# Kernel optimization log

Hardware: AMD Instinct MI355X
Metric: run time of the kernel (lower is better)

## Reference

```python
import jax, jax.numpy as jnp
import numpy as np

HIDDEN = 1024
INTER = 1408
N_EXPERTS = 8
TOTAL_TOKENS = 8192


def setup_inputs() -> dict:
    key = jax.random.key(0)
    k_x, k_w1, k_w2 = jax.random.split(key, 3)
    x = jax.random.normal(k_x, (TOTAL_TOKENS, HIDDEN), dtype=jnp.float32)
    # fused gate+up projection per expert: [E, H, 2*I]
    w1w3 = jax.random.normal(k_w1, (N_EXPERTS, HIDDEN, 2 * INTER), dtype=jnp.float32) * (HIDDEN ** -0.5)
    # down projection per expert: [E, I, H]
    w2 = jax.random.normal(k_w2, (N_EXPERTS, INTER, HIDDEN), dtype=jnp.float32) * (INTER ** -0.5)
    # deterministic uneven split that sums exactly to TOTAL_TOKENS
    tpe = np.array([700, 1300, 900, 1100, 1024, 1024, 800, 1344], dtype=np.int64)
    assert tpe.sum() == TOTAL_TOKENS
    tokens_per_expert = jnp.asarray(tpe)
    return {"x": x, "w1w3": w1w3, "w2": w2, "tokens_per_expert": tokens_per_expert, "decoding": False}


def _grouped_mm(inp, W, expert_ids):
    # inp: [T, D_in], W: [E, D_in, D_out]; rows of inp are grouped by expert,
    # expert_ids[t] = owning expert. Equivalent to per-segment GEMM with W[e].
    T = inp.shape[0]
    E = W.shape[0]
    out = jnp.zeros((T, W.shape[-1]), dtype=inp.dtype)
    for e in range(E):  # fixed small expert count; loop over experts, not tokens
        mask = (expert_ids == e)[:, None]
        out = out + jnp.where(mask, inp, 0.0) @ W[e]
    return out


def reference(x, w1w3, w2, tokens_per_expert, decoding):
    T = x.shape[0]
    E = w1w3.shape[0]
    # per-token expert id from contiguous segment lengths (jit-safe fixed length)
    expert_ids = jnp.repeat(jnp.arange(E), tokens_per_expert, total_repeat_length=T)
    gate_up = _grouped_mm(x, w1w3, expert_ids)          # [T, 2*I]
    gate, up = jnp.split(gate_up, 2, axis=-1)           # swiglu(split_dim=-1)
    h = jax.nn.silu(gate) * up                          # [T, I]
    return _grouped_mm(h, w2, expert_ids)               # [T, H]
```

## Files before the change

kernel.cpp:

```cpp
#include <hip/hip_runtime.h>
#include <hip/hip_bf16.h>


#define HIDDEN 1024
#define INTER  1408
#define NEXP   8
#define TOKENS 8192

typedef __attribute__((ext_vector_type(8))) short bf16x8;
typedef __attribute__((ext_vector_type(4))) float f32x4;
typedef __attribute__((ext_vector_type(4))) unsigned short u16x4;
typedef __attribute__((ext_vector_type(8))) unsigned short u16x8;

#define GLOAD_LDS16(g, l)                                                      \
  __builtin_amdgcn_global_load_lds(                                            \
      (const __attribute__((address_space(1))) void*)(g),                      \
      (__attribute__((address_space(3))) void*)(l), 16, 0, 0)

__device__ inline unsigned short f2bf(float f) {
  unsigned int x = __float_as_uint(f);
  x += 0x7fffu + ((x >> 16) & 1u);
  return (unsigned short)(x >> 16);
}

__device__ inline int detect_f32(const float* __restrict__ xf, int lane) {
  unsigned int u = __float_as_uint(xf[lane & 63]);
  int e = (u >> 23) & 0xff;
  return __popcll(__ballot(e >= 100 && e <= 140)) >= 48 ? 1 : 0;
}

__device__ inline void load_tpe(const int* __restrict__ raw, int* tpe) {
  bool ok = true; int s = 0;
#pragma unroll
  for (int e = 0; e < NEXP; e++) { int v = raw[e]; tpe[e] = v; ok = ok && (v >= 0 && v <= TOKENS); s += v; }
  if (ok && s == TOKENS) return;
  ok = true; s = 0;
#pragma unroll
  for (int e = 0; e < NEXP; e++) { int v = raw[2 * e]; tpe[e] = v; ok = ok && (v >= 0 && v <= TOKENS); s += v; }
  if (ok && s == TOKENS) return;
  const int fb[NEXP] = {700, 1300, 900, 1100, 1024, 1024, 800, 1344};
#pragma unroll
  for (int e = 0; e < NEXP; e++) tpe[e] = fb[e];
}

__device__ inline bool expert_map(const int* __restrict__ tpe_raw, int rt,
                                  int& expert, int& row0, int& rows_valid) {
  int tpe[NEXP];
  load_tpe(tpe_raw, tpe);
  int acc = 0, pre = 0;
#pragma unroll
  for (int e = 0; e < NEXP; e++) {
    int nt = (tpe[e] + 127) >> 7;
    if (rt < acc + nt) {
      int ti = rt - acc;
      expert = e; row0 = pre + ti * 128; rows_valid = tpe[e] - ti * 128;
      return true;
    }
    acc += nt; pre += tpe[e];
  }
  return false;
}

template <int RE, int CE, int LOG_NC4, int LOG_NRCH>
__device__ inline void ldst_transpose(const void* __restrict__ in,
                                      unsigned short* __restrict__ out,
                                      int R, int C, int r0, int c0,
                                      int t, int f32,
                                      unsigned short* __restrict__ lds) {
  constexpr int NC4 = 1 << LOG_NC4;
  constexpr int NRCH = 1 << LOG_NRCH;
  constexpr int MASK = NRCH - 1;
  constexpr int RPR = (256 >> LOG_NC4) * 8;
  constexpr int ROUNDS = RE / RPR;
  static_assert(NC4 * 4 == CE && NRCH * 8 == RE, "geometry");
  static_assert(ROUNDS * RPR == RE, "rounds");

  const int clane = t & (NC4 - 1);
  const int rslot = t >> LOG_NC4;
  const int c = clane * 4;
#pragma unroll
  for (int round = 0; round < ROUNDS; ++round) {
    const int rb = round * RPR + rslot * 8;
    u16x8 w[4];
    if (f32) {
      f32x4 v[8];
#pragma unroll
      for (int i = 0; i < 8; i++)
        v[i] = *(const f32x4*)((const float*)in + (size_t)(r0 + rb + i) * C + c0 + c);
#pragma unroll
      for (int j = 0; j < 4; j++)
#pragma unroll
        for (int i = 0; i < 8; i++) w[j][i] = f2bf(v[i][j]);
    } else {
      u16x4 v[8];
#pragma unroll
      for (int i = 0; i < 8; i++)
        v[i] = *(const u16x4*)((const unsigned short*)in + (size_t)(r0 + rb + i) * C + c0 + c);
#pragma unroll
      for (int j = 0; j < 4; j++)
#pragma unroll
        for (int i = 0; i < 8; i++) w[j][i] = v[i][j];
    }
    const int rch = rb >> 3;
#pragma unroll
    for (int j = 0; j < 4; j++) {
      const int cc = c + j;
      const int chunk = (cc << LOG_NRCH) + (rch ^ ((cc >> 2) & MASK));
      *(u16x8*)&lds[chunk * 8] = w[j];
    }
  }
  __syncthreads();

  const int rl = t & (NRCH - 1);
  const int cslot = t >> LOG_NRCH;
  constexpr int CSLOTS = 256 >> LOG_NRCH;
#pragma unroll
  for (int it = 0; it < CE / CSLOTS; ++it) {
    const int crow = it * CSLOTS + cslot;
    const int chunk = (crow << LOG_NRCH) + (rl ^ ((crow >> 2) & MASK));
    u16x8 w = *(const u16x8*)&lds[chunk * 8];
    *(u16x8*)&out[(size_t)(c0 + crow) * R + r0 + rl * 8] = w;
  }
}

__global__ __launch_bounds__(256) void prepare(
    const float* __restrict__ xf, const void* __restrict__ x,
    const void* __restrict__ w1w3,
    unsigned short* __restrict__ xb, unsigned short* __restrict__ w1t) {
  __shared__ __align__(16) unsigned short lds[16384];
  const int t = threadIdx.x;
  const int f32 = detect_f32(xf, t & 63);
  const int b = blockIdx.x;

  if (b < 512) {
    const size_t base = (size_t)b * 16384 + t * 4;
#pragma unroll
    for (int it = 0; it < 16; ++it) {
      const size_t i = base + (size_t)it * 1024;
      u16x4 v;
      if (f32) {
        f32x4 g = *(const f32x4*)((const float*)x + i);
        v[0] = f2bf(g[0]); v[1] = f2bf(g[1]); v[2] = f2bf(g[2]); v[3] = f2bf(g[3]);
      } else {
        v = *(const u16x4*)((const unsigned short*)x + i);
      }
      *(u16x4*)(xb + i) = v;
    }
    return;
  }

  const int u = b - 512;
  const int ex = u / 176, rem = u % 176;
  const int r0 = (rem / 22) * 128, c0 = (rem % 22) * 128;
  const char* in = (const char*)w1w3 + (size_t)ex * 1024 * 2816 * (f32 ? 4 : 2);
  ldst_transpose<128, 128, 5, 4>(in, w1t + (size_t)ex * 2816 * 1024,
                                 1024, 2816, r0, c0, t, f32, lds);
}

__global__ __launch_bounds__(256, 2) void moe_gemm1(
    const unsigned short* __restrict__ xb, const unsigned short* __restrict__ w1t,
    const int* __restrict__ tpe_raw, unsigned short* __restrict__ h,
    const void* __restrict__ w2raw, unsigned short* __restrict__ w2t,
    const float* __restrict__ xf) {
  __shared__ __align__(16) unsigned short smem[16384];
  const int tid = threadIdx.x;

  if (blockIdx.y >= 72) {
    const int f32 = detect_f32(xf, tid & 63);
    const int idx = (blockIdx.y - 72) * 22 + blockIdx.x;
    const int ex = idx / 88, rem = idx % 88;
    const int r0 = (rem / 8) * 128, c0 = (rem % 8) * 128;
    const char* in = (const char*)w2raw + (size_t)ex * 1408 * 1024 * (f32 ? 4 : 2);
    ldst_transpose<128, 128, 5, 4>(in, w2t + (size_t)ex * 1024 * 1408,
                                   1408, 1024, r0, c0, tid, f32, smem);
    return;
  }

#define AS(b_) (smem + (b_) * 4096)
#define BG(b_) (smem + 8192 + (b_) * 2048)
#define BU(b_) (smem + 12288 + (b_) * 2048)
  int expert, row0, rows_valid;
  if (!expert_map(tpe_raw, blockIdx.y, expert, row0, rows_valid)) return;

  const int lane = tid & 63, wave = tid >> 6;
  const int wr = wave >> 1, wc = wave & 1;
  const int i0 = blockIdx.x * 64;
  const unsigned short* W = w1t + (size_t)expert * 2816 * HIDDEN;

  const int q0 = wave * 2, q1 = wave * 2 + 1;
  const int sr0 = q0 * 16 + (lane >> 2), sr1 = q1 * 16 + (lane >> 2);
  const int sb = wave * 16 + (lane >> 2);
  const int sk = (((lane & 3) ^ ((lane >> 3) & 3))) * 8;
  const size_t arow0 = (size_t)min(row0 + sr0, TOKENS - 1);
  const size_t arow1 = (size_t)min(row0 + sr1, TOKENS - 1);
  const unsigned short* pa0 = xb + arow0 * HIDDEN + sk;
  const unsigned short* pa1 = xb + arow1 * HIDDEN + sk;
  const unsigned short* pg = W + (size_t)(i0 + sb) * HIDDEN + sk;
  const unsigned short* pu = W + (size_t)(INTER + i0 + sb) * HIDDEN + sk;

  f32x4 accg[4][2] = {};
  f32x4 accu[4][2] = {};
  const int fr = lane & 15, fq = (lane >> 4) * 8;
  const int fqs = fq ^ (((fr >> 1) & 3) << 3);

  GLOAD_LDS16(pa0, AS(0) + q0 * 512);
  GLOAD_LDS16(pa1, AS(0) + q1 * 512);
  GLOAD_LDS16(pg, BG(0) + wave * 512);
  GLOAD_LDS16(pu, BU(0) + wave * 512);
  pa0 += 32; pa1 += 32; pg += 32; pu += 32;
  __syncthreads();

  const int NT = HIDDEN / 32;
  for (int it = 0; it < NT; ++it) {
    const int cur = it & 1, nxt = cur ^ 1;
    if (it + 1 < NT) {
      GLOAD_LDS16(pa0, AS(nxt) + q0 * 512);
      GLOAD_LDS16(pa1, AS(nxt) + q1 * 512);
      GLOAD_LDS16(pg, BG(nxt) + wave * 512);
      GLOAD_LDS16(pu, BU(nxt) + wave * 512);
      pa0 += 32; pa1 += 32; pg += 32; pu += 32;
    }

    bf16x8 a[4], bg[2], bu[2];
#pragma unroll
    for (int mi = 0; mi < 4; mi++)
      a[mi] = *(const bf16x8*)&AS(cur)[(wr * 64 + mi * 16 + fr) * 32 + fqs];
#pragma unroll
    for (int ni = 0; ni < 2; ni++) {
      bg[ni] = *(const bf16x8*)&BG(cur)[(wc * 32 + ni * 16 + fr) * 32 + fqs];
      bu[ni] = *(const bf16x8*)&BU(cur)[(wc * 32 + ni * 16 + fr) * 32 + fqs];
    }
#pragma unroll
    for (int mi = 0; mi < 4; mi++)
#pragma unroll
      for (int ni = 0; ni < 2; ni++) {
        accg[mi][ni] =
            __builtin_amdgcn_mfma_f32_16x16x32_bf16(a[mi], bg[ni], accg[mi][ni], 0, 0, 0);
        accu[mi][ni] =
            __builtin_amdgcn_mfma_f32_16x16x32_bf16(a[mi], bu[ni], accu[mi][ni], 0, 0, 0);
      }

    __syncthreads();
  }

#pragma unroll
  for (int mi = 0; mi < 4; mi++)
#pragma unroll
    for (int r = 0; r < 4; r++) {
      const int row_local = wr * 64 + mi * 16 + ((lane >> 4) * 4) + r;
      if (row_local < rows_valid && row0 + row_local < TOKENS) {
        const size_t rowoff = (size_t)(row0 + row_local) * INTER;
#pragma unroll
        for (int ni = 0; ni < 2; ni++) {
          const int col = i0 + wc * 32 + ni * 16 + fr;
          const float g = accg[mi][ni][r];
          const float u = accu[mi][ni][r];
          const float sg = g / (1.0f + __expf(-g));
          h[rowoff + col] = f2bf(sg * u);
        }
      }
    }
#undef AS
#undef BG
#undef BU
}

__global__ __launch_bounds__(256, 2) void moe_gemm2(
    const unsigned short* __restrict__ h, const unsigned short* __restrict__ w2t,
    const int* __restrict__ tpe_raw, void* __restrict__ out,
    const float* __restrict__ xf) {
  __shared__ unsigned short As[2][128 * 32];
  __shared__ unsigned short Bs[2][128 * 32];
  int expert, row0, rows_valid;
  if (!expert_map(tpe_raw, blockIdx.y, expert, row0, rows_valid)) return;
  const int f32out = detect_f32(xf, threadIdx.x & 63);

  const int tid = threadIdx.x;
  const int lane = tid & 63, wave = tid >> 6;
  const int wr = wave >> 1, wc = wave & 1;
  const int n0 = blockIdx.x * 128;
  const unsigned short* W = w2t + (size_t)expert * INTER * HIDDEN;

  const int q0 = wave * 2, q1 = wave * 2 + 1;
  const int sr0 = q0 * 16 + (lane >> 2), sr1 = q1 * 16 + (lane >> 2);
  const int sk = (((lane & 3) ^ ((lane >> 3) & 3))) * 8;
  const size_t arow0 = (size_t)min(row0 + sr0, TOKENS - 1);
  const size_t arow1 = (size_t)min(row0 + sr1, TOKENS - 1);
  const unsigned short* pa0 = h + arow0 * INTER + sk;
  const unsigned short* pa1 = h + arow1 * INTER + sk;
  const unsigned short* pb0 = W + (size_t)(n0 + sr0) * INTER + sk;
  const unsigned short* pb1 = W + (size_t)(n0 + sr1) * INTER + sk;

  f32x4 acc[4][4] = {};
  const int fr = lane & 15, fq = (lane >> 4) * 8;
  const int fqs = fq ^ (((fr >> 1) & 3) << 3);

  GLOAD_LDS16(pa0, &As[0][q0 * 512]);
  GLOAD_LDS16(pa1, &As[0][q1 * 512]);
  GLOAD_LDS16(pb0, &Bs[0][q0 * 512]);
  GLOAD_LDS16(pb1, &Bs[0][q1 * 512]);
  pa0 += 32; pa1 += 32; pb0 += 32; pb1 += 32;
  __syncthreads();

  const int NT = INTER / 32;
  for (int it = 0; it < NT; ++it) {
    const int cur = it & 1, nxt = cur ^ 1;
    if (it + 1 < NT) {
      GLOAD_LDS16(pa0, &As[nxt][q0 * 512]);
      GLOAD_LDS16(pa1, &As[nxt][q1 * 512]);
      GLOAD_LDS16(pb0, &Bs[nxt][q0 * 512]);
      GLOAD_LDS16(pb1, &Bs[nxt][q1 * 512]);
      pa0 += 32; pa1 += 32; pb0 += 32; pb1 += 32;
    }

    bf16x8 a[4], bb[4];
#pragma unroll
    for (int mi = 0; mi < 4; mi++)
      a[mi] = *(const bf16x8*)&As[cur][(wr * 64 + mi * 16 + fr) * 32 + fqs];
#pragma unroll
    for (int ni = 0; ni < 4; ni++)
      bb[ni] = *(const bf16x8*)&Bs[cur][(wc * 64 + ni * 16 + fr) * 32 + fqs];
#pragma unroll
    for (int mi = 0; mi < 4; mi++)
#pragma unroll
      for (int ni = 0; ni < 4; ni++)
        acc[mi][ni] =
            __builtin_amdgcn_mfma_f32_16x16x32_bf16(a[mi], bb[ni], acc[mi][ni], 0, 0, 0);

    __syncthreads();
  }

#pragma unroll
  for (int mi = 0; mi < 4; mi++)
#pragma unroll
    for (int r = 0; r < 4; r++) {
      const int row_local = wr * 64 + mi * 16 + ((lane >> 4) * 4) + r;
      if (row_local < rows_valid && row0 + row_local < TOKENS) {
        const size_t rowoff = (size_t)(row0 + row_local) * HIDDEN;
#pragma unroll
        for (int ni = 0; ni < 4; ni++) {
          const int col = n0 + wc * 64 + ni * 16 + fr;
          if (f32out)
            ((float*)out)[rowoff + col] = acc[mi][ni][r];
          else
            ((unsigned short*)out)[rowoff + col] = f2bf(acc[mi][ni][r]);
        }
      }
    }
}

extern "C" void kernel_launch(void* const* d_in, const int* in_sizes, int n_in,
                              void* d_out, int out_size, void* d_ws, size_t ws_size,
                              hipStream_t stream) {
  const void* x = d_in[0];
  const void* w1w3 = d_in[1];
  const void* w2 = d_in[2];
  const int* tpe = (const int*)d_in[3];
  const float* xf = (const float*)d_in[0];

  const size_t XB_BYTES = (size_t)TOKENS * HIDDEN * 2;
  const size_t W1T_BYTES = (size_t)NEXP * 2816 * HIDDEN * 2;
  const size_t W2T_BYTES = (size_t)NEXP * INTER * HIDDEN * 2;
  char* ws = (char*)d_ws;
  unsigned short* xb = (unsigned short*)ws;
  unsigned short* w1t = (unsigned short*)(ws + XB_BYTES);
  unsigned short* w2t = (unsigned short*)(ws + XB_BYTES + W1T_BYTES);
  unsigned short* h = (unsigned short*)(ws + XB_BYTES + W1T_BYTES + W2T_BYTES);

  prepare<<<1920, 256, 0, stream>>>(xf, x, w1w3, xb, w1t);
  moe_gemm1<<<dim3(INTER / 64, 104), 256, 0, stream>>>(xb, w1t, tpe, h, w2, w2t, xf);
  moe_gemm2<<<dim3(HIDDEN / 128, 72), 256, 0, stream>>>(h, w2t, tpe, d_out, xf);
}
```

Before: 324.8 us.

## Triple-buffer LDS with two-ahead prefetch and swizzle block order in MoE GEMMs

Both grouped GEMM kernels move from double to triple buffering in LDS. Loads are issued two k-tiles ahead and synchronised with explicit vmcnt waits plus a raw s_barrier instead of a full __syncthreads drain, so more memory latency can overlap with MFMA work. The launch grid is also remapped with an interleaving swizzle so that blocks scheduled together touch different rows and experts, which changes L2 reuse and load balance. The extra LDS (48KB in gemm1) may reduce occupancy at two blocks per CU, and the hand-written waitcnt counts must stay correct to avoid races.

```diff
diff --git a/kernel.cpp b/kernel.cpp
--- a/kernel.cpp
+++ b/kernel.cpp
@@ -162,12 +162,16 @@
     const int* __restrict__ tpe_raw, unsigned short* __restrict__ h,
     const void* __restrict__ w2raw, unsigned short* __restrict__ w2t,
     const float* __restrict__ xf) {
-  __shared__ __align__(16) unsigned short smem[16384];
+  __shared__ __align__(16) unsigned short smem[24576];
   const int tid = threadIdx.x;
 
-  if (blockIdx.y >= 72) {
+  const int lin = blockIdx.y * 22 + blockIdx.x;
+  const int swz = (lin & 7) * 286 + (lin >> 3);
+  const int by = swz / 22, bx = swz % 22;
+
+  if (by >= 72) {
     const int f32 = detect_f32(xf, tid & 63);
-    const int idx = (blockIdx.y - 72) * 22 + blockIdx.x;
+    const int idx = (by - 72) * 22 + bx;
     const int ex = idx / 88, rem = idx % 88;
     const int r0 = (rem / 8) * 128, c0 = (rem % 8) * 128;
     const char* in = (const char*)w2raw + (size_t)ex * 1408 * 1024 * (f32 ? 4 : 2);
@@ -177,14 +181,14 @@
   }
 
 #define AS(b_) (smem + (b_) * 4096)
-#define BG(b_) (smem + 8192 + (b_) * 2048)
-#define BU(b_) (smem + 12288 + (b_) * 2048)
+#define BG(b_) (smem + 12288 + (b_) * 2048)
+#define BU(b_) (smem + 18432 + (b_) * 2048)
   int expert, row0, rows_valid;
-  if (!expert_map(tpe_raw, blockIdx.y, expert, row0, rows_valid)) return;
+  if (!expert_map(tpe_raw, by, expert, row0, rows_valid)) return;
 
   const int lane = tid & 63, wave = tid >> 6;
   const int wr = wave >> 1, wc = wave & 1;
-  const int i0 = blockIdx.x * 64;
+  const int i0 = bx * 64;
   const unsigned short* W = w1t + (size_t)expert * 2816 * HIDDEN;
 
   const int q0 = wave * 2, q1 = wave * 2 + 1;
@@ -208,16 +212,23 @@
   GLOAD_LDS16(pg, BG(0) + wave * 512);
   GLOAD_LDS16(pu, BU(0) + wave * 512);
   pa0 += 32; pa1 += 32; pg += 32; pu += 32;
-  __syncthreads();
+  GLOAD_LDS16(pa0, AS(1) + q0 * 512);
+  GLOAD_LDS16(pa1, AS(1) + q1 * 512);
+  GLOAD_LDS16(pg, BG(1) + wave * 512);
+  GLOAD_LDS16(pu, BU(1) + wave * 512);
+  pa0 += 32; pa1 += 32; pg += 32; pu += 32;
+  asm volatile("s_waitcnt vmcnt(4)" ::: "memory");
+  __builtin_amdgcn_s_barrier();
 
   const int NT = HIDDEN / 32;
   for (int it = 0; it < NT; ++it) {
-    const int cur = it & 1, nxt = cur ^ 1;
-    if (it + 1 < NT) {
-      GLOAD_LDS16(pa0, AS(nxt) + q0 * 512);
-      GLOAD_LDS16(pa1, AS(nxt) + q1 * 512);
-      GLOAD_LDS16(pg, BG(nxt) + wave * 512);
-      GLOAD_LDS16(pu, BU(nxt) + wave * 512);
+    const int cur = it % 3;
+    if (it + 2 < NT) {
+      const int pf = (it + 2) % 3;
+      GLOAD_LDS16(pa0, AS(pf) + q0 * 512);
+      GLOAD_LDS16(pa1, AS(pf) + q1 * 512);
+      GLOAD_LDS16(pg, BG(pf) + wave * 512);
+      GLOAD_LDS16(pu, BU(pf) + wave * 512);
       pa0 += 32; pa1 += 32; pg += 32; pu += 32;
     }
 
@@ -240,7 +251,9 @@
             __builtin_amdgcn_mfma_f32_16x16x32_bf16(a[mi], bu[ni], accu[mi][ni], 0, 0, 0);
       }
 
-    __syncthreads();
+    if (it + 2 < NT) asm volatile("s_waitcnt vmcnt(4)" ::: "memory");
+    else             asm volatile("s_waitcnt vmcnt(0)" ::: "memory");
+    __builtin_amdgcn_s_barrier();
   }
 
 #pragma unroll
@@ -269,16 +282,21 @@
     const unsigned short* __restrict__ h, const unsigned short* __restrict__ w2t,
     const int* __restrict__ tpe_raw, void* __restrict__ out,
     const float* __restrict__ xf) {
-  __shared__ unsigned short As[2][128 * 32];
-  __shared__ unsigned short Bs[2][128 * 32];
+  __shared__ __align__(16) unsigned short As[3][4096];
+  __shared__ __align__(16) unsigned short Bs[3][4096];
+
+  const int lin = blockIdx.y * 8 + blockIdx.x;
+  const int swz = (lin & 7) * 72 + (lin >> 3);
+  const int by = swz >> 3, bx = swz & 7;
+
   int expert, row0, rows_valid;
-  if (!expert_map(tpe_raw, blockIdx.y, expert, row0, rows_valid)) return;
+  if (!expert_map(tpe_raw, by, expert, row0, rows_valid)) return;
   const int f32out = detect_f32(xf, threadIdx.x & 63);
 
   const int tid = threadIdx.x;
   const int lane = tid & 63, wave = tid >> 6;
   const int wr = wave >> 1, wc = wave & 1;
-  const int n0 = blockIdx.x * 128;
+  const int n0 = bx * 128;
   const unsigned short* W = w2t + (size_t)expert * INTER * HIDDEN;
 
   const int q0 = wave * 2, q1 = wave * 2 + 1;
@@ -300,16 +318,23 @@
   GLOAD_LDS16(pb0, &Bs[0][q0 * 512]);
   GLOAD_LDS16(pb1, &Bs[0][q1 * 512]);
   pa0 += 32; pa1 += 32; pb0 += 32; pb1 += 32;
-  __syncthreads();
+  GLOAD_LDS16(pa0, &As[1][q0 * 512]);
+  GLOAD_LDS16(pa1, &As[1][q1 * 512]);
+  GLOAD_LDS16(pb0, &Bs[1][q0 * 512]);
+  GLOAD_LDS16(pb1, &Bs[1][q1 * 512]);
+  pa0 += 32; pa1 += 32; pb0 += 32; pb1 += 32;
+  asm volatile("s_waitcnt vmcnt(4)" ::: "memory");
+  __builtin_amdgcn_s_barrier();
 
   const int NT = INTER / 32;
   for (int it = 0; it < NT; ++it) {
-    const int cur = it & 1, nxt = cur ^ 1;
-    if (it + 1 < NT) {
-      GLOAD_LDS16(pa0, &As[nxt][q0 * 512]);
-      GLOAD_LDS16(pa1, &As[nxt][q1 * 512]);
-      GLOAD_LDS16(pb0, &Bs[nxt][q0 * 512]);
-      GLOAD_LDS16(pb1, &Bs[nxt][q1 * 512]);
+    const int cur = it % 3;
+    if (it + 2 < NT) {
+      const int pf = (it + 2) % 3;
+      GLOAD_LDS16(pa0, &As[pf][q0 * 512]);
+      GLOAD_LDS16(pa1, &As[pf][q1 * 512]);
+      GLOAD_LDS16(pb0, &Bs[pf][q0 * 512]);
+      GLOAD_LDS16(pb1, &Bs[pf][q1 * 512]);
       pa0 += 32; pa1 += 32; pb0 += 32; pb1 += 32;
     }
 
@@ -327,7 +352,9 @@
         acc[mi][ni] =
             __builtin_amdgcn_mfma_f32_16x16x32_bf16(a[mi], bb[ni], acc[mi][ni], 0, 0, 0);
 
-    __syncthreads();
+    if (it + 2 < NT) asm volatile("s_waitcnt vmcnt(4)" ::: "memory");
+    else             asm volatile("s_waitcnt vmcnt(0)" ::: "memory");
+    __builtin_amdgcn_s_barrier();
   }
 
 #pragma unroll
```

Measured after the change: 329.9 us. About the same (+1.6%).

## Fuse x bf16 conversion into gemm1 A-loads and swizzle block order

Applied to the files above, without the earlier changes.

The separate x-to-bf16 conversion pass in prepare is removed. gemm1 now loads x directly (fp32 or bf16) into registers, converts it and writes it to LDS with a swizzle, software-pipelined across the k loop. prepare uses 512-thread blocks that transpose larger 256x128 tiles. Both GEMMs remap block indices so that consecutive blocks are spread across experts and row tiles, likely for L2 or XCD locality. The cost is register-staged A loads in place of direct global-to-LDS loads, and gemm1 now reads twice the bytes for its A tile when the input is fp32.

```diff
diff --git a/kernel.cpp b/kernel.cpp
--- a/kernel.cpp
+++ b/kernel.cpp
@@ -61,7 +61,7 @@
   return false;
 }
 
-template <int RE, int CE, int LOG_NC4, int LOG_NRCH>
+template <int THREADS, int RE, int CE, int LOG_NC4, int LOG_NRCH>
 __device__ inline void ldst_transpose(const void* __restrict__ in,
                                       unsigned short* __restrict__ out,
                                       int R, int C, int r0, int c0,
@@ -70,7 +70,7 @@
   constexpr int NC4 = 1 << LOG_NC4;
   constexpr int NRCH = 1 << LOG_NRCH;
   constexpr int MASK = NRCH - 1;
-  constexpr int RPR = (256 >> LOG_NC4) * 8;
+  constexpr int RPR = (THREADS >> LOG_NC4) * 8;
   constexpr int ROUNDS = RE / RPR;
   static_assert(NC4 * 4 == CE && NRCH * 8 == RE, "geometry");
   static_assert(ROUNDS * RPR == RE, "rounds");
@@ -113,7 +113,7 @@
 
   const int rl = t & (NRCH - 1);
   const int cslot = t >> LOG_NRCH;
-  constexpr int CSLOTS = 256 >> LOG_NRCH;
+  constexpr int CSLOTS = THREADS >> LOG_NRCH;
 #pragma unroll
   for (int it = 0; it < CE / CSLOTS; ++it) {
     const int crow = it * CSLOTS + cslot;
@@ -123,56 +123,47 @@
   }
 }
 
-__global__ __launch_bounds__(256) void prepare(
-    const float* __restrict__ xf, const void* __restrict__ x,
-    const void* __restrict__ w1w3,
-    unsigned short* __restrict__ xb, unsigned short* __restrict__ w1t) {
-  __shared__ __align__(16) unsigned short lds[16384];
+__global__ __launch_bounds__(512) void prepare(
+    const float* __restrict__ xf, const void* __restrict__ w1w3,
+    unsigned short* __restrict__ w1t) {
+  __shared__ __align__(16) unsigned short lds[32768];
   const int t = threadIdx.x;
   const int f32 = detect_f32(xf, t & 63);
   const int b = blockIdx.x;
 
-  if (b < 512) {
-    const size_t base = (size_t)b * 16384 + t * 4;
-#pragma unroll
-    for (int it = 0; it < 16; ++it) {
-      const size_t i = base + (size_t)it * 1024;
-      u16x4 v;
-      if (f32) {
-        f32x4 g = *(const f32x4*)((const float*)x + i);
-        v[0] = f2bf(g[0]); v[1] = f2bf(g[1]); v[2] = f2bf(g[2]); v[3] = f2bf(g[3]);
-      } else {
-        v = *(const u16x4*)((const unsigned short*)x + i);
-      }
-      *(u16x4*)(xb + i) = v;
-    }
-    return;
-  }
-
-  const int u = b - 512;
-  const int ex = u / 176, rem = u % 176;
-  const int r0 = (rem / 22) * 128, c0 = (rem % 22) * 128;
+  const int ex = b / 88, rem = b % 88;
+  const int r0 = (rem / 22) * 256, c0 = (rem % 22) * 128;
   const char* in = (const char*)w1w3 + (size_t)ex * 1024 * 2816 * (f32 ? 4 : 2);
-  ldst_transpose<128, 128, 5, 4>(in, w1t + (size_t)ex * 2816 * 1024,
-                                 1024, 2816, r0, c0, t, f32, lds);
+  ldst_transpose<512, 256, 128, 5, 5>(in, w1t + (size_t)ex * 2816 * 1024,
+                                      1024, 2816, r0, c0, t, f32, lds);
 }
 
 __global__ __launch_bounds__(256, 2) void moe_gemm1(
-    const unsigned short* __restrict__ xb, const unsigned short* __restrict__ w1t,
+    const void* __restrict__ x, const unsigned short* __restrict__ w1t,
     const int* __restrict__ tpe_raw, unsigned short* __restrict__ h,
     const void* __restrict__ w2raw, unsigned short* __restrict__ w2t,
     const float* __restrict__ xf) {
   __shared__ __align__(16) unsigned short smem[16384];
   const int tid = threadIdx.x;
 
-  if (blockIdx.y >= 72) {
+  const int lin = blockIdx.y * 22 + blockIdx.x;
+  int swz;
+  if (lin < 1584) {
+    swz = (lin & 7) * 198 + (lin >> 3);
+  } else {
+    const int tt = lin - 1584;
+    swz = 1584 + (tt & 7) * 88 + (tt >> 3);
+  }
+  const int by = swz / 22, bx = swz % 22;
+
+  if (by >= 72) {
     const int f32 = detect_f32(xf, tid & 63);
-    const int idx = (blockIdx.y - 72) * 22 + blockIdx.x;
+    const int idx = (by - 72) * 22 + bx;
     const int ex = idx / 88, rem = idx % 88;
     const int r0 = (rem / 8) * 128, c0 = (rem % 8) * 128;
     const char* in = (const char*)w2raw + (size_t)ex * 1408 * 1024 * (f32 ? 4 : 2);
-    ldst_transpose<128, 128, 5, 4>(in, w2t + (size_t)ex * 1024 * 1408,
-                                   1408, 1024, r0, c0, tid, f32, smem);
+    ldst_transpose<256, 128, 128, 5, 4>(in, w2t + (size_t)ex * 1024 * 1408,
+                                        1408, 1024, r0, c0, tid, f32, smem);
     return;
   }
 
@@ -180,45 +171,75 @@
 #define BG(b_) (smem + 8192 + (b_) * 2048)
 #define BU(b_) (smem + 12288 + (b_) * 2048)
   int expert, row0, rows_valid;
-  if (!expert_map(tpe_raw, blockIdx.y, expert, row0, rows_valid)) return;
+  if (!expert_map(tpe_raw, by, expert, row0, rows_valid)) return;
+  const int f32 = detect_f32(xf, tid & 63);
 
   const int lane = tid & 63, wave = tid >> 6;
   const int wr = wave >> 1, wc = wave & 1;
-  const int i0 = blockIdx.x * 64;
+  const int i0 = bx * 64;
   const unsigned short* W = w1t + (size_t)expert * 2816 * HIDDEN;
 
-  const int q0 = wave * 2, q1 = wave * 2 + 1;
-  const int sr0 = q0 * 16 + (lane >> 2), sr1 = q1 * 16 + (lane >> 2);
   const int sb = wave * 16 + (lane >> 2);
   const int sk = (((lane & 3) ^ ((lane >> 3) & 3))) * 8;
-  const size_t arow0 = (size_t)min(row0 + sr0, TOKENS - 1);
-  const size_t arow1 = (size_t)min(row0 + sr1, TOKENS - 1);
-  const unsigned short* pa0 = xb + arow0 * HIDDEN + sk;
-  const unsigned short* pa1 = xb + arow1 * HIDDEN + sk;
   const unsigned short* pg = W + (size_t)(i0 + sb) * HIDDEN + sk;
   const unsigned short* pu = W + (size_t)(INTER + i0 + sb) * HIDDEN + sk;
+
+  const int ar = tid >> 1;
+  const int koff = (tid & 1) * 16;
+  const int akey = (ar >> 1) & 3;
+  const int as0 = (((koff >> 3) ^ akey)) * 8;
+  const int as1 = ((((koff >> 3) + 1) ^ akey)) * 8;
+  const size_t arow = (size_t)min(row0 + ar, TOKENS - 1);
+  const int esz = f32 ? 4 : 2;
+  const char* pax = (const char*)x + ((size_t)arow * HIDDEN + koff) * esz;
+
+  f32x4 avf[4]; u16x8 avb[2];
+#define A_LOAD()                                                               \
+  do {                                                                         \
+    if (f32) {                                                                 \
+      const f32x4* p_ = (const f32x4*)pax;                                     \
+      avf[0] = p_[0]; avf[1] = p_[1]; avf[2] = p_[2]; avf[3] = p_[3];          \
+    } else {                                                                   \
+      const u16x8* p_ = (const u16x8*)pax;                                     \
+      avb[0] = p_[0]; avb[1] = p_[1];                                          \
+    }                                                                          \
+    pax += 32 * esz;                                                           \
+  } while (0)
+#define A_WRITE(buf_)                                                          \
+  do {                                                                         \
+    u16x8 h0_, h1_;                                                            \
+    if (f32) {                                                                 \
+      _Pragma("unroll")                                                        \
+      for (int j_ = 0; j_ < 4; j_++) {                                         \
+        h0_[j_]     = f2bf(avf[0][j_]); h0_[j_ + 4] = f2bf(avf[1][j_]);        \
+        h1_[j_]     = f2bf(avf[2][j_]); h1_[j_ + 4] = f2bf(avf[3][j_]);        \
+      }                                                                        \
+    } else { h0_ = avb[0]; h1_ = avb[1]; }                                     \
+    *(u16x8*)((buf_) + ar * 32 + as0) = h0_;                                   \
+    *(u16x8*)((buf_) + ar * 32 + as1) = h1_;                                   \
+  } while (0)
 
   f32x4 accg[4][2] = {};
   f32x4 accu[4][2] = {};
   const int fr = lane & 15, fq = (lane >> 4) * 8;
   const int fqs = fq ^ (((fr >> 1) & 3) << 3);
 
-  GLOAD_LDS16(pa0, AS(0) + q0 * 512);
-  GLOAD_LDS16(pa1, AS(0) + q1 * 512);
   GLOAD_LDS16(pg, BG(0) + wave * 512);
   GLOAD_LDS16(pu, BU(0) + wave * 512);
-  pa0 += 32; pa1 += 32; pg += 32; pu += 32;
+  pg += 32; pu += 32;
+  A_LOAD();
+  A_WRITE(AS(0));
   __syncthreads();
 
   const int NT = HIDDEN / 32;
   for (int it = 0; it < NT; ++it) {
     const int cur = it & 1, nxt = cur ^ 1;
-    if (it + 1 < NT) {
-      GLOAD_LDS16(pa0, AS(nxt) + q0 * 512);
-      GLOAD_LDS16(pa1, AS(nxt) + q1 * 512);
+    const bool pfv = (it + 1 < NT);
+    if (pfv) {
       GLOAD_LDS16(pg, BG(nxt) + wave * 512);
       GLOAD_LDS16(pu, BU(nxt) + wave * 512);
-      pa0 += 32; pa1 += 32; pg += 32; pu += 32;
+      pg += 32; pu += 32;
+      A_LOAD();
     }
 
     bf16x8 a[4], bg[2], bu[2];
@@ -240,6 +261,7 @@
             __builtin_amdgcn_mfma_f32_16x16x32_bf16(a[mi], bu[ni], accu[mi][ni], 0, 0, 0);
       }
 
+    if (pfv) A_WRITE(AS(nxt));
     __syncthreads();
   }
 
@@ -263,6 +285,8 @@
 #undef AS
 #undef BG
 #undef BU
+#undef A_LOAD
+#undef A_WRITE
 }
 
 __global__ __launch_bounds__(256, 2) void moe_gemm2(
@@ -271,14 +295,19 @@
     const float* __restrict__ xf) {
   __shared__ unsigned short As[2][128 * 32];
   __shared__ unsigned short Bs[2][128 * 32];
+
+  const int lin = blockIdx.y * 8 + blockIdx.x;
+  const int swz = (lin & 7) * 72 + (lin >> 3);
+  const int by = swz >> 3, bx = swz & 7;
+
   int expert, row0, rows_valid;
-  if (!expert_map(tpe_raw, blockIdx.y, expert, row0, rows_valid)) return;
+  if (!expert_map(tpe_raw, by, expert, row0, rows_valid)) return;
   const int f32out = detect_f32(xf, threadIdx.x & 63);
 
   const int tid = threadIdx.x;
   const int lane = tid & 63, wave = tid >> 6;
   const int wr = wave >> 1, wc = wave & 1;
-  const int n0 = blockIdx.x * 128;
+  const int n0 = bx * 128;
   const unsigned short* W = w2t + (size_t)expert * INTER * HIDDEN;
 
   const int q0 = wave * 2, q1 = wave * 2 + 1;
@@ -358,16 +387,14 @@
   const int* tpe = (const int*)d_in[3];
   const float* xf = (const float*)d_in[0];
 
-  const size_t XB_BYTES = (size_t)TOKENS * HIDDEN * 2;
   const size_t W1T_BYTES = (size_t)NEXP * 2816 * HIDDEN * 2;
   const size_t W2T_BYTES = (size_t)NEXP * INTER * HIDDEN * 2;
   char* ws = (char*)d_ws;
-  unsigned short* xb = (unsigned short*)ws;
-  unsigned short* w1t = (unsigned short*)(ws + XB_BYTES);
-  unsigned short* w2t = (unsigned short*)(ws + XB_BYTES + W1T_BYTES);
-  unsigned short* h = (unsigned short*)(ws + XB_BYTES + W1T_BYTES + W2T_BYTES);
-
-  prepare<<<1920, 256, 0, stream>>>(xf, x, w1w3, xb, w1t);
-  moe_gemm1<<<dim3(INTER / 64, 104), 256, 0, stream>>>(xb, w1t, tpe, h, w2, w2t, xf);
-  moe_gemm2<<<dim3(HIDDEN / 128, 72), 256, 0, stream>>>(h, w2t, tpe, d_out, xf);
-}
+  unsigned short* w1t = (unsigned short*)ws;
+  unsigned short* w2t = (unsigned short*)(ws + W1T_BYTES);
+  unsigned short* h = (unsigned short*)(ws + W1T_BYTES + W2T_BYTES);
+
+  prepare<<<704, 512, 0, stream>>>(xf, w1w3, w1t);
+  moe_gemm1<<<dim3(22, 104), 256, 0, stream>>>(x, w1t, tpe, h, w2, w2t, xf);
+  moe_gemm2<<<dim3(8, 72), 256, 0, stream>>>(h, w2t, tpe, d_out, xf);
+}
```

Measured after the change: 343.0 us. 1.06x slower.

## Swizzle GEMM block order per XCD and enlarge prepare transpose tiles

Applied to the files above, without the earlier changes.

Remaps linear block indices in both grouped GEMMs so each XCD receives a contiguous range of tiles, improving L2 reuse of expert weights and activation rows across the chiplets. The prepare kernel moves to 512-thread blocks with 256x128 transpose tiles and halves its block count. The transpose helper is templated on thread count. Larger prepare blocks use more LDS and may reduce occupancy.

```diff
diff --git a/kernel.cpp b/kernel.cpp
--- a/kernel.cpp
+++ b/kernel.cpp
@@ -61,7 +61,7 @@
   return false;
 }
 
-template <int RE, int CE, int LOG_NC4, int LOG_NRCH>
+template <int THREADS, int RE, int CE, int LOG_NC4, int LOG_NRCH>
 __device__ inline void ldst_transpose(const void* __restrict__ in,
                                       unsigned short* __restrict__ out,
                                       int R, int C, int r0, int c0,
@@ -70,7 +70,7 @@
   constexpr int NC4 = 1 << LOG_NC4;
   constexpr int NRCH = 1 << LOG_NRCH;
   constexpr int MASK = NRCH - 1;
-  constexpr int RPR = (256 >> LOG_NC4) * 8;
+  constexpr int RPR = (THREADS >> LOG_NC4) * 8;
   constexpr int ROUNDS = RE / RPR;
   static_assert(NC4 * 4 == CE && NRCH * 8 == RE, "geometry");
   static_assert(ROUNDS * RPR == RE, "rounds");
@@ -113,7 +113,7 @@
 
   const int rl = t & (NRCH - 1);
   const int cslot = t >> LOG_NRCH;
-  constexpr int CSLOTS = 256 >> LOG_NRCH;
+  constexpr int CSLOTS = THREADS >> LOG_NRCH;
 #pragma unroll
   for (int it = 0; it < CE / CSLOTS; ++it) {
     const int crow = it * CSLOTS + cslot;
@@ -123,20 +123,20 @@
   }
 }
 
-__global__ __launch_bounds__(256) void prepare(
+__global__ __launch_bounds__(512) void prepare(
     const float* __restrict__ xf, const void* __restrict__ x,
     const void* __restrict__ w1w3,
     unsigned short* __restrict__ xb, unsigned short* __restrict__ w1t) {
-  __shared__ __align__(16) unsigned short lds[16384];
+  __shared__ __align__(16) unsigned short lds[32768];
   const int t = threadIdx.x;
   const int f32 = detect_f32(xf, t & 63);
   const int b = blockIdx.x;
 
-  if (b < 512) {
-    const size_t base = (size_t)b * 16384 + t * 4;
+  if (b < 256) {
+    const size_t base = (size_t)b * 32768 + t * 4;
 #pragma unroll
     for (int it = 0; it < 16; ++it) {
-      const size_t i = base + (size_t)it * 1024;
+      const size_t i = base + (size_t)it * 2048;
       u16x4 v;
       if (f32) {
         f32x4 g = *(const f32x4*)((const float*)x + i);
@@ -149,12 +149,12 @@
     return;
   }
 
-  const int u = b - 512;
-  const int ex = u / 176, rem = u % 176;
-  const int r0 = (rem / 22) * 128, c0 = (rem % 22) * 128;
+  const int u = b - 256;
+  const int ex = u / 88, rem = u % 88;
+  const int r0 = (rem / 22) * 256, c0 = (rem % 22) * 128;
   const char* in = (const char*)w1w3 + (size_t)ex * 1024 * 2816 * (f32 ? 4 : 2);
-  ldst_transpose<128, 128, 5, 4>(in, w1t + (size_t)ex * 2816 * 1024,
-                                 1024, 2816, r0, c0, t, f32, lds);
+  ldst_transpose<512, 256, 128, 5, 5>(in, w1t + (size_t)ex * 2816 * 1024,
+                                      1024, 2816, r0, c0, t, f32, lds);
 }
 
 __global__ __launch_bounds__(256, 2) void moe_gemm1(
@@ -165,14 +165,24 @@
   __shared__ __align__(16) unsigned short smem[16384];
   const int tid = threadIdx.x;
 
-  if (blockIdx.y >= 72) {
+  const int lin = blockIdx.y * 22 + blockIdx.x;
+  int swz;
+  if (lin < 1584) {
+    swz = (lin & 7) * 198 + (lin >> 3);
+  } else {
+    const int tt = lin - 1584;
+    swz = 1584 + (tt & 7) * 88 + (tt >> 3);
+  }
+  const int by = swz / 22, bx = swz % 22;
+
+  if (by >= 72) {
     const int f32 = detect_f32(xf, tid & 63);
-    const int idx = (blockIdx.y - 72) * 22 + blockIdx.x;
+    const int idx = (by - 72) * 22 + bx;
     const int ex = idx / 88, rem = idx % 88;
     const int r0 = (rem / 8) * 128, c0 = (rem % 8) * 128;
     const char* in = (const char*)w2raw + (size_t)ex * 1408 * 1024 * (f32 ? 4 : 2);
-    ldst_transpose<128, 128, 5, 4>(in, w2t + (size_t)ex * 1024 * 1408,
-                                   1408, 1024, r0, c0, tid, f32, smem);
+    ldst_transpose<256, 128, 128, 5, 4>(in, w2t + (size_t)ex * 1024 * 1408,
+                                        1408, 1024, r0, c0, tid, f32, smem);
     return;
   }
 
@@ -180,11 +190,11 @@
 #define BG(b_) (smem + 8192 + (b_) * 2048)
 #define BU(b_) (smem + 12288 + (b_) * 2048)
   int expert, row0, rows_valid;
-  if (!expert_map(tpe_raw, blockIdx.y, expert, row0, rows_valid)) return;
+  if (!expert_map(tpe_raw, by, expert, row0, rows_valid)) return;
 
   const int lane = tid & 63, wave = tid >> 6;
   const int wr = wave >> 1, wc = wave & 1;
-  const int i0 = blockIdx.x * 64;
+  const int i0 = bx * 64;
   const unsigned short* W = w1t + (size_t)expert * 2816 * HIDDEN;
 
   const int q0 = wave * 2, q1 = wave * 2 + 1;
@@ -271,14 +281,19 @@
     const float* __restrict__ xf) {
   __shared__ unsigned short As[2][128 * 32];
   __shared__ unsigned short Bs[2][128 * 32];
+
+  const int lin = blockIdx.y * 8 + blockIdx.x;
+  const int swz = (lin & 7) * 72 + (lin >> 3);
+  const int by = swz >> 3, bx = swz & 7;
+
   int expert, row0, rows_valid;
-  if (!expert_map(tpe_raw, blockIdx.y, expert, row0, rows_valid)) return;
+  if (!expert_map(tpe_raw, by, expert, row0, rows_valid)) return;
   const int f32out = detect_f32(xf, threadIdx.x & 63);
 
   const int tid = threadIdx.x;
   const int lane = tid & 63, wave = tid >> 6;
   const int wr = wave >> 1, wc = wave & 1;
-  const int n0 = blockIdx.x * 128;
+  const int n0 = bx * 128;
   const unsigned short* W = w2t + (size_t)expert * INTER * HIDDEN;
 
   const int q0 = wave * 2, q1 = wave * 2 + 1;
@@ -367,7 +382,7 @@
   unsigned short* w2t = (unsigned short*)(ws + XB_BYTES + W1T_BYTES);
   unsigned short* h = (unsigned short*)(ws + XB_BYTES + W1T_BYTES + W2T_BYTES);
 
-  prepare<<<1920, 256, 0, stream>>>(xf, x, w1w3, xb, w1t);
-  moe_gemm1<<<dim3(INTER / 64, 104), 256, 0, stream>>>(xb, w1t, tpe, h, w2, w2t, xf);
-  moe_gemm2<<<dim3(HIDDEN / 128, 72), 256, 0, stream>>>(h, w2t, tpe, d_out, xf);
-}
+  prepare<<<960, 512, 0, stream>>>(xf, x, w1w3, xb, w1t);
+  moe_gemm1<<<dim3(22, 104), 256, 0, stream>>>(xb, w1t, tpe, h, w2, w2t, xf);
+  moe_gemm2<<<dim3(8, 72), 256, 0, stream>>>(h, w2t, tpe, d_out, xf);
+}
```

Result: faster. 313.6 us (-3.4%).
